# Optimization experiments

Hardware: AMD Instinct MI355X
Metric: run time of the kernel (lower is better)

## Reference

```python
import jax, jax.numpy as jnp
import numpy as np

H = 8  # num_heads
LN_EPS = 1e-5


def setup_inputs() -> dict:
    key = jax.random.key(0)
    ks = jax.random.split(key, 12)
    B, N, D = 1, 4096, 256
    E = 65536
    x = jax.random.normal(ks[0], (B, N, D), dtype=jnp.float32)
    # random edges + self-loops so every row of the mask has >=1 True (avoids NaN softmax)
    src = jax.random.randint(ks[1], (E,), 0, N)
    dst = jax.random.randint(ks[2], (E,), 0, N)
    loop = jnp.arange(N)
    edge_index = jnp.stack([jnp.concatenate([src, loop]),
                            jnp.concatenate([dst, loop])]).astype(jnp.int64)  # [2, 69632]
    s = 1.0 / np.sqrt(D)
    Wq = jax.random.normal(ks[3], (D, D), dtype=jnp.float32) * s
    Wk = jax.random.normal(ks[4], (D, D), dtype=jnp.float32) * s
    Wv = jax.random.normal(ks[5], (D, D), dtype=jnp.float32) * s
    Wo = jax.random.normal(ks[6], (D, D), dtype=jnp.float32) * s
    bq = jax.random.normal(ks[7], (D,), dtype=jnp.float32) * 0.01
    bk = jax.random.normal(ks[8], (D,), dtype=jnp.float32) * 0.01
    bv = jax.random.normal(ks[9], (D,), dtype=jnp.float32) * 0.01
    bo = jax.random.normal(ks[10], (D,), dtype=jnp.float32) * 0.01
    gamma = jnp.ones((D,), dtype=jnp.float32)
    beta = jnp.zeros((D,), dtype=jnp.float32)
    return {"x": x, "edge_index": edge_index, "Wq": Wq, "bq": bq, "Wk": Wk, "bk": bk,
            "Wv": Wv, "bv": bv, "Wo": Wo, "bo": bo, "gamma": gamma, "beta": beta}


def reference(x, edge_index, Wq, bq, Wk, bk, Wv, bv, Wo, bo, gamma, beta):
    B, N, D = x.shape
    hd = D // H
    # QKV projections -> [B, H, N, hd]
    def proj(W, b):
        return (x @ W + b).reshape(B, N, H, hd).transpose(0, 2, 1, 3)
    Q, K, V = proj(Wq, bq), proj(Wk, bk), proj(Wv, bv)
    scores = jnp.einsum('bhnd,bhmd->bhnm', Q, K) / jnp.sqrt(jnp.float32(hd))
    # dense boolean adjacency mask scattered from edge list
    mask = jnp.zeros((N, N), dtype=bool).at[edge_index[0], edge_index[1]].set(True)
    scores = jnp.where(mask[None, None], scores, -jnp.inf)
    attn = jax.nn.softmax(scores, axis=-1)  # dropout is identity in eval mode
    attended = jnp.einsum('bhnm,bhmd->bhnd', attn, V)
    attended = attended.transpose(0, 2, 1, 3).reshape(B, N, D)
    out = attended @ Wo + bo
    y = x + out
    mu = jnp.mean(y, axis=-1, keepdims=True)
    var = jnp.mean((y - mu) ** 2, axis=-1, keepdims=True)
    return (y - mu) / jnp.sqrt(var + LN_EPS) * gamma + beta
```

## Files before the change

kernel.cpp:

```cpp
#include <hip/hip_runtime.h>

#define N_NODES 4096
#define DMODEL  256
#define NHEAD   8
#define HDIM    32
#define LN_EPS  1e-5f
#define MAXDEG  64

typedef __attribute__((ext_vector_type(8))) short short8;
typedef __attribute__((ext_vector_type(4))) float f32x4;

__device__ __forceinline__ unsigned short f2bf(float f) {
  unsigned int x = __float_as_uint(f);
  x += 0x7fffu + ((x >> 16) & 1u);
  return (unsigned short)(x >> 16);
}
__device__ __forceinline__ float bf2f(unsigned short u) {
  return __uint_as_float(((unsigned int)u) << 16);
}

__device__ __forceinline__ int wt_off(int n, int k) {
  return ((k >> 5) * 4 + ((k >> 3) & 3)) * 2048 + n * 8 + (k & 7);
}

__global__ __launch_bounds__(256) void prep_kernel(
    const float* __restrict__ w0, const float* __restrict__ w1,
    const float* __restrict__ w2, const float* __restrict__ w3,
    unsigned short* __restrict__ wt,
    const int* __restrict__ e0, const int* __restrict__ e1, int ne, int eb,
    unsigned int* __restrict__ bits, int* __restrict__ cnt) {
  __shared__ float t[32][33];
  int bid = blockIdx.x, tid = threadIdx.x;
  if (bid < 256) {
    int kbi = bid & 7, nbi = (bid >> 3) & 7, m = bid >> 6;
    const float* w = (m == 0) ? w0 : (m == 1) ? w1 : (m == 2) ? w2 : w3;
    int tx = tid & 31, ty = tid >> 5;
    int kb = kbi * 32, nb = nbi * 32;
#pragma unroll
    for (int r = 0; r < 32; r += 8)
      t[ty + r][tx] = w[(kb + ty + r) * 256 + nb + tx];
    __syncthreads();
    unsigned short* o = wt + m * 65536;
#pragma unroll
    for (int r = 0; r < 32; r += 8)
      o[(kbi * 4 + (tx >> 3)) * 2048 + (nb + ty + r) * 8 + (tx & 7)] =
          f2bf(t[tx][ty + r]);
  } else if (bid < 256 + eb) {
    int i = (bid - 256) * 256 + tid;
    if (i < ne) {
      unsigned int bitpos = ((unsigned int)e0[i] << 12) | (unsigned int)e1[i];
      bits[bitpos >> 5] = 0u;
    }
  } else {
    cnt[(bid - 256 - eb) * 256 + tid] = 0;
  }
}

__global__ __launch_bounds__(512) void qkv_scatter(
    const float* __restrict__ x, const unsigned short* __restrict__ wt,
    const float* __restrict__ bq, const float* __restrict__ bk,
    const float* __restrict__ bv,
    const int* __restrict__ e0, const int* __restrict__ e1, int ne,
    unsigned int* __restrict__ bits, int* __restrict__ cnt,
    int* __restrict__ colidx,
    unsigned short* __restrict__ Qb, unsigned short* __restrict__ Kb,
    unsigned short* __restrict__ Vb) {
  int bid = blockIdx.x, tid = threadIdx.x;
  if (bid >= 256) {
    int i = (bid - 256) * 512 + tid;
    if (i < ne) {
      int s = e0[i], d = e1[i];
      unsigned int bitpos = ((unsigned int)s << 12) | (unsigned int)d;
      unsigned int word = bitpos >> 5, msk = 1u << (bitpos & 31);
      unsigned int old = atomicOr(&bits[word], msk);
      if (!(old & msk)) {
        int pos = atomicAdd(&cnt[s], 1);
        if (pos < MAXDEG) colidx[s * MAXDEG + pos] = d;
      }
    }
    return;
  }
  int lane = tid & 63, w = tid >> 6;
  int Mbase = bid * 16;
  int arow = lane & 15, kgrp = lane >> 4;
  short8 a[8];
  const float* ab = x + (Mbase + arow) * 256 + kgrp * 8;
#pragma unroll
  for (int kk = 0; kk < 8; ++kk) {
    float4 v0 = *reinterpret_cast<const float4*>(ab + kk * 32);
    float4 v1 = *reinterpret_cast<const float4*>(ab + kk * 32 + 4);
    short8 tv;
    tv[0] = (short)f2bf(v0.x); tv[1] = (short)f2bf(v0.y);
    tv[2] = (short)f2bf(v0.z); tv[3] = (short)f2bf(v0.w);
    tv[4] = (short)f2bf(v1.x); tv[5] = (short)f2bf(v1.y);
    tv[6] = (short)f2bf(v1.z); tv[7] = (short)f2bf(v1.w);
    a[kk] = tv;
  }
#pragma unroll
  for (int mat = 0; mat < 3; ++mat) {
    const unsigned short* wm = wt + mat * 65536;
    const float* bias_p = (mat == 0) ? bq : (mat == 1) ? bk : bv;
    unsigned short* o = (mat == 0) ? Qb : (mat == 1) ? Kb : Vb;
#pragma unroll
    for (int nf = 0; nf < 2; ++nf) {
      int col = w * 32 + nf * 16 + arow;
      const unsigned short* bb = wm + kgrp * 2048 + col * 8;
      f32x4 acc = {0.f, 0.f, 0.f, 0.f};
#pragma unroll
      for (int kk = 0; kk < 8; ++kk) {
        short8 b = *reinterpret_cast<const short8*>(bb + kk * 8192);
        acc = __builtin_amdgcn_mfma_f32_16x16x32_bf16(a[kk], b, acc, 0, 0, 0);
      }
      float bias = bias_p[col];
#pragma unroll
      for (int r = 0; r < 4; ++r) {
        int row = Mbase + kgrp * 4 + r;
        o[row * 256 + col] = f2bf(acc[r] + bias);
      }
    }
  }
}

__global__ __launch_bounds__(1024, 1) void attn_out_ln(
    const unsigned short* __restrict__ Qb, const unsigned short* __restrict__ Kb,
    const unsigned short* __restrict__ Vb, const int* __restrict__ cnt,
    const int* __restrict__ colidx, const unsigned short* __restrict__ wot,
    const float* __restrict__ bo, const float* __restrict__ x,
    const float* __restrict__ gamma, const float* __restrict__ beta,
    float* __restrict__ out) {
  __shared__ unsigned short att_lds[16][264];
  __shared__ float ylds[16][260];
  __shared__ float ps[16][65], pq[16][65];
  __shared__ float mu_s[16], ri_s[16];

  int tid = threadIdx.x;
  int Mbase = blockIdx.x * 16;
  const float scale = 0.17677669529663687f;

  {
    int g = tid >> 3;
    int gl = tid & 7;
    int ni = g >> 3, h = g & 7;
    int n = Mbase + ni;

    float qf[32];
    {
      const short8* q8 = reinterpret_cast<const short8*>(Qb + n * 256 + h * 32);
#pragma unroll
      for (int b = 0; b < 4; ++b) {
        short8 qv = q8[b];
#pragma unroll
        for (int j = 0; j < 8; ++j) qf[b * 8 + j] = bf2f((unsigned short)qv[j]) * scale;
      }
    }

    int deg = cnt[n]; deg = (deg > MAXDEG) ? MAXDEG : deg;
    const int* nbrs = colidx + n * MAXDEG;

    float s[8]; int c[8];
#pragma unroll
    for (int i = 0; i < 8; ++i) { s[i] = -3.0e38f; c[i] = 0; }
#pragma unroll
    for (int i = 0; i < 8; ++i) {
      if (8 * i >= deg) break;
      int idx = 8 * i + gl;
      if (idx < deg) {
        c[i] = nbrs[idx];
        const short8* k8 = reinterpret_cast<const short8*>(Kb + c[i] * 256 + h * 32);
        float d = 0.f;
#pragma unroll
        for (int b = 0; b < 4; ++b) {
          short8 kv = k8[b];
#pragma unroll
          for (int j = 0; j < 8; ++j)
            d += qf[b * 8 + j] * bf2f((unsigned short)kv[j]);
        }
        s[i] = d;
      }
    }

    float gm = s[0];
#pragma unroll
    for (int i = 1; i < 8; ++i) gm = fmaxf(gm, s[i]);
    gm = fmaxf(gm, __shfl_xor(gm, 1, 8));
    gm = fmaxf(gm, __shfl_xor(gm, 2, 8));
    gm = fmaxf(gm, __shfl_xor(gm, 4, 8));

    float l = 0.f;
#pragma unroll
    for (int i = 0; i < 8; ++i) {
      if (8 * i >= deg) break;
      s[i] = __expf(s[i] - gm);
      l += s[i];
    }
    l += __shfl_xor(l, 1, 8);
    l += __shfl_xor(l, 2, 8);
    l += __shfl_xor(l, 4, 8);

    float a0 = 0.f, a1 = 0.f, a2 = 0.f, a3 = 0.f;
#pragma unroll
    for (int i = 0; i < 8; ++i) {
      if (8 * i >= deg) break;
#pragma unroll
      for (int lj = 0; lj < 8; ++lj) {
        if (8 * i + lj >= deg) break;
        float pj = __shfl(s[i], lj, 8);
        int cj = __shfl(c[i], lj, 8);
        ushort4 vv = *reinterpret_cast<const ushort4*>(Vb + cj * 256 + h * 32 + gl * 4);
        a0 += pj * bf2f(vv.x);
        a1 += pj * bf2f(vv.y);
        a2 += pj * bf2f(vv.z);
        a3 += pj * bf2f(vv.w);
      }
    }
    float rl = 1.f / l;
    ushort4 pkt;
    pkt.x = f2bf(a0 * rl); pkt.y = f2bf(a1 * rl);
    pkt.z = f2bf(a2 * rl); pkt.w = f2bf(a3 * rl);
    *reinterpret_cast<ushort4*>(&att_lds[ni][h * 32 + gl * 4]) = pkt;
  }
  __syncthreads();

  {
    int lane = tid & 63, w = tid >> 6;
    int arow = lane & 15, kgrp = lane >> 4;

    short8 a[8];
#pragma unroll
    for (int kk = 0; kk < 8; ++kk)
      a[kk] = *reinterpret_cast<const short8*>(&att_lds[arow][kgrp * 8 + kk * 32]);

    int col = w * 16 + arow;
    const unsigned short* bb = wot + kgrp * 2048 + col * 8;
    f32x4 acc = {0.f, 0.f, 0.f, 0.f};
#pragma unroll
    for (int kk = 0; kk < 8; ++kk) {
      short8 b = *reinterpret_cast<const short8*>(bb + kk * 8192);
      acc = __builtin_amdgcn_mfma_f32_16x16x32_bf16(a[kk], b, acc, 0, 0, 0);
    }
    float bof = bo[col];
#pragma unroll
    for (int r = 0; r < 4; ++r) {
      int row = kgrp * 4 + r;
      float xv = x[(Mbase + row) * 256 + col];
      ylds[row][col] = acc[r] + bof + xv;
    }
  }
  __syncthreads();

  int r = tid >> 6, seg = tid & 63;
  float sm = 0.f, sq = 0.f;
#pragma unroll
  for (int j = 0; j < 4; ++j) {
    float v = ylds[r][seg * 4 + j];
    sm += v;
    sq += v * v;
  }
  ps[r][seg] = sm;
  pq[r][seg] = sq;
  __syncthreads();
  if (tid < 16) {
    float S = 0.f, Q2 = 0.f;
#pragma unroll
    for (int cc = 0; cc < 64; ++cc) { S += ps[tid][cc]; Q2 += pq[tid][cc]; }
    float mu = S * (1.f / 256.f);
    float var = Q2 * (1.f / 256.f) - mu * mu;
    mu_s[tid] = mu;
    ri_s[tid] = rsqrtf(var + LN_EPS);
  }
  __syncthreads();
  float mu = mu_s[r], ri = ri_s[r];
  float* orow = out + (Mbase + r) * 256;
#pragma unroll
  for (int j = 0; j < 4; ++j) {
    int cc = seg * 4 + j;
    float v = (ylds[r][cc] - mu) * ri * gamma[cc] + beta[cc];
    orow[cc] = v;
  }
}

extern "C" void kernel_launch(void* const* d_in, const int* in_sizes, int n_in,
                              void* d_out, int out_size, void* d_ws, size_t ws_size,
                              hipStream_t stream) {
  const float* x     = (const float*)d_in[0];
  const int*   edges = (const int*)d_in[1];
  const float* Wq    = (const float*)d_in[2];
  const float* bq    = (const float*)d_in[3];
  const float* Wk    = (const float*)d_in[4];
  const float* bk    = (const float*)d_in[5];
  const float* Wv    = (const float*)d_in[6];
  const float* bv    = (const float*)d_in[7];
  const float* Wo    = (const float*)d_in[8];
  const float* bo    = (const float*)d_in[9];
  const float* gamma = (const float*)d_in[10];
  const float* beta  = (const float*)d_in[11];
  float* out = (float*)d_out;
  int NE = in_sizes[1] / 2;
  int EB256 = (NE + 255) / 256;
  int EB512 = (NE + 511) / 512;

  char* p = (char*)d_ws;
  auto carve = [&](size_t sz) { char* r = p; p += ((sz + 255) / 256) * 256; return r; };
  unsigned short* Wt   = (unsigned short*)carve(4 * 65536 * sizeof(unsigned short));
  unsigned short* Qb   = (unsigned short*)carve((size_t)N_NODES * DMODEL * sizeof(unsigned short));
  unsigned short* Kb   = (unsigned short*)carve((size_t)N_NODES * DMODEL * sizeof(unsigned short));
  unsigned short* Vb   = (unsigned short*)carve((size_t)N_NODES * DMODEL * sizeof(unsigned short));
  unsigned int*   bits = (unsigned int*)carve((size_t)N_NODES * N_NODES / 8);
  int*            cnt  = (int*)carve(N_NODES * sizeof(int));
  int*            colidx = (int*)carve((size_t)N_NODES * MAXDEG * sizeof(int));

  prep_kernel<<<256 + EB256 + 16, 256, 0, stream>>>(Wq, Wk, Wv, Wo, Wt,
                                                    edges, edges + NE, NE, EB256, bits, cnt);
  qkv_scatter<<<256 + EB512, 512, 0, stream>>>(x, Wt, bq, bk, bv,
                                               edges, edges + NE, NE, bits, cnt, colidx,
                                               Qb, Kb, Vb);
  attn_out_ln<<<256, 1024, 0, stream>>>(Qb, Kb, Vb, cnt, colidx, Wt + 3 * 65536,
                                        bo, x, gamma, beta, out);
}
```

Baseline: 48.88 us.

## Fuse three kernels into one persistent kernel with grid-wide barriers

Merges the weight-transpose/clear, QKV projection plus edge scatter, and attention plus output projection plus LayerNorm kernels into a single 256-block launch. Grid-wide atomic counter barriers separate the stages, and a memset resets the counter before launch. This removes two kernel launch gaps and their tail effects. In exchange it depends on all 256 blocks being co-resident, and the per-block work is redistributed, with each wave now computing one column tile per matrix.

Result: slower. 124.6 us (+155.0%).

```diff
diff --git a/kernel.cpp b/kernel.cpp
--- a/kernel.cpp
+++ b/kernel.cpp
@@ -19,263 +19,267 @@
   return __uint_as_float(((unsigned int)u) << 16);
 }
 
-__device__ __forceinline__ int wt_off(int n, int k) {
-  return ((k >> 5) * 4 + ((k >> 3) & 3)) * 2048 + n * 8 + (k & 7);
-}
-
-__global__ __launch_bounds__(256) void prep_kernel(
-    const float* __restrict__ w0, const float* __restrict__ w1,
-    const float* __restrict__ w2, const float* __restrict__ w3,
-    unsigned short* __restrict__ wt,
-    const int* __restrict__ e0, const int* __restrict__ e1, int ne, int eb,
-    unsigned int* __restrict__ bits, int* __restrict__ cnt) {
+__device__ __forceinline__ void gbar(unsigned int* ctr, unsigned int target) {
+  __syncthreads();
+  if (threadIdx.x == 0) {
+    __threadfence();
+    __hip_atomic_fetch_add(ctr, 1u, __ATOMIC_SEQ_CST, __HIP_MEMORY_SCOPE_AGENT);
+    while (__hip_atomic_load(ctr, __ATOMIC_SEQ_CST, __HIP_MEMORY_SCOPE_AGENT) < target)
+      __builtin_amdgcn_s_sleep(8);
+    __threadfence();
+  }
+  __syncthreads();
+}
+
+__global__ __launch_bounds__(1024, 1) void fused_all(
+    const float* __restrict__ x, const int* __restrict__ edges, int ne,
+    const float* __restrict__ Wq, const float* __restrict__ bq,
+    const float* __restrict__ Wk, const float* __restrict__ bk,
+    const float* __restrict__ Wv, const float* __restrict__ bv,
+    const float* __restrict__ Wo, const float* __restrict__ bo,
+    const float* __restrict__ gamma, const float* __restrict__ beta,
+    unsigned short* wt, unsigned short* Qb, unsigned short* Kb,
+    unsigned short* Vb, unsigned int* bits, int* cnt, int* colidx,
+    unsigned int* ctr, float* __restrict__ out) {
   __shared__ float t[32][33];
-  int bid = blockIdx.x, tid = threadIdx.x;
-  if (bid < 256) {
-    int kbi = bid & 7, nbi = (bid >> 3) & 7, m = bid >> 6;
-    const float* w = (m == 0) ? w0 : (m == 1) ? w1 : (m == 2) ? w2 : w3;
-    int tx = tid & 31, ty = tid >> 5;
-    int kb = kbi * 32, nb = nbi * 32;
-#pragma unroll
-    for (int r = 0; r < 32; r += 8)
-      t[ty + r][tx] = w[(kb + ty + r) * 256 + nb + tx];
-    __syncthreads();
-    unsigned short* o = wt + m * 65536;
-#pragma unroll
-    for (int r = 0; r < 32; r += 8)
-      o[(kbi * 4 + (tx >> 3)) * 2048 + (nb + ty + r) * 8 + (tx & 7)] =
-          f2bf(t[tx][ty + r]);
-  } else if (bid < 256 + eb) {
-    int i = (bid - 256) * 256 + tid;
-    if (i < ne) {
-      unsigned int bitpos = ((unsigned int)e0[i] << 12) | (unsigned int)e1[i];
-      bits[bitpos >> 5] = 0u;
-    }
-  } else {
-    cnt[(bid - 256 - eb) * 256 + tid] = 0;
-  }
-}
-
-__global__ __launch_bounds__(512) void qkv_scatter(
-    const float* __restrict__ x, const unsigned short* __restrict__ wt,
-    const float* __restrict__ bq, const float* __restrict__ bk,
-    const float* __restrict__ bv,
-    const int* __restrict__ e0, const int* __restrict__ e1, int ne,
-    unsigned int* __restrict__ bits, int* __restrict__ cnt,
-    int* __restrict__ colidx,
-    unsigned short* __restrict__ Qb, unsigned short* __restrict__ Kb,
-    unsigned short* __restrict__ Vb) {
-  int bid = blockIdx.x, tid = threadIdx.x;
-  if (bid >= 256) {
-    int i = (bid - 256) * 512 + tid;
-    if (i < ne) {
-      int s = e0[i], d = e1[i];
-      unsigned int bitpos = ((unsigned int)s << 12) | (unsigned int)d;
-      unsigned int word = bitpos >> 5, msk = 1u << (bitpos & 31);
-      unsigned int old = atomicOr(&bits[word], msk);
-      if (!(old & msk)) {
-        int pos = atomicAdd(&cnt[s], 1);
-        if (pos < MAXDEG) colidx[s * MAXDEG + pos] = d;
-      }
-    }
-    return;
-  }
-  int lane = tid & 63, w = tid >> 6;
-  int Mbase = bid * 16;
-  int arow = lane & 15, kgrp = lane >> 4;
-  short8 a[8];
-  const float* ab = x + (Mbase + arow) * 256 + kgrp * 8;
-#pragma unroll
-  for (int kk = 0; kk < 8; ++kk) {
-    float4 v0 = *reinterpret_cast<const float4*>(ab + kk * 32);
-    float4 v1 = *reinterpret_cast<const float4*>(ab + kk * 32 + 4);
-    short8 tv;
-    tv[0] = (short)f2bf(v0.x); tv[1] = (short)f2bf(v0.y);
-    tv[2] = (short)f2bf(v0.z); tv[3] = (short)f2bf(v0.w);
-    tv[4] = (short)f2bf(v1.x); tv[5] = (short)f2bf(v1.y);
-    tv[6] = (short)f2bf(v1.z); tv[7] = (short)f2bf(v1.w);
-    a[kk] = tv;
-  }
-#pragma unroll
-  for (int mat = 0; mat < 3; ++mat) {
-    const unsigned short* wm = wt + mat * 65536;
-    const float* bias_p = (mat == 0) ? bq : (mat == 1) ? bk : bv;
-    unsigned short* o = (mat == 0) ? Qb : (mat == 1) ? Kb : Vb;
-#pragma unroll
-    for (int nf = 0; nf < 2; ++nf) {
-      int col = w * 32 + nf * 16 + arow;
-      const unsigned short* bb = wm + kgrp * 2048 + col * 8;
-      f32x4 acc = {0.f, 0.f, 0.f, 0.f};
-#pragma unroll
-      for (int kk = 0; kk < 8; ++kk) {
-        short8 b = *reinterpret_cast<const short8*>(bb + kk * 8192);
-        acc = __builtin_amdgcn_mfma_f32_16x16x32_bf16(a[kk], b, acc, 0, 0, 0);
-      }
-      float bias = bias_p[col];
-#pragma unroll
-      for (int r = 0; r < 4; ++r) {
-        int row = Mbase + kgrp * 4 + r;
-        o[row * 256 + col] = f2bf(acc[r] + bias);
-      }
-    }
-  }
-}
-
-__global__ __launch_bounds__(1024, 1) void attn_out_ln(
-    const unsigned short* __restrict__ Qb, const unsigned short* __restrict__ Kb,
-    const unsigned short* __restrict__ Vb, const int* __restrict__ cnt,
-    const int* __restrict__ colidx, const unsigned short* __restrict__ wot,
-    const float* __restrict__ bo, const float* __restrict__ x,
-    const float* __restrict__ gamma, const float* __restrict__ beta,
-    float* __restrict__ out) {
   __shared__ unsigned short att_lds[16][264];
   __shared__ float ylds[16][260];
   __shared__ float ps[16][65], pq[16][65];
   __shared__ float mu_s[16], ri_s[16];
 
-  int tid = threadIdx.x;
-  int Mbase = blockIdx.x * 16;
+  const int tid = threadIdx.x;
+  const int bid = blockIdx.x;
+  const int* e0 = edges;
+  const int* e1 = edges + ne;
   const float scale = 0.17677669529663687f;
 
   {
-    int g = tid >> 3;
-    int gl = tid & 7;
-    int ni = g >> 3, h = g & 7;
-    int n = Mbase + ni;
-
-    float qf[32];
-    {
-      const short8* q8 = reinterpret_cast<const short8*>(Qb + n * 256 + h * 32);
-#pragma unroll
-      for (int b = 0; b < 4; ++b) {
-        short8 qv = q8[b];
-#pragma unroll
-        for (int j = 0; j < 8; ++j) qf[b * 8 + j] = bf2f((unsigned short)qv[j]) * scale;
-      }
-    }
-
-    int deg = cnt[n]; deg = (deg > MAXDEG) ? MAXDEG : deg;
-    const int* nbrs = colidx + n * MAXDEG;
-
-    float s[8]; int c[8];
-#pragma unroll
-    for (int i = 0; i < 8; ++i) { s[i] = -3.0e38f; c[i] = 0; }
-#pragma unroll
-    for (int i = 0; i < 8; ++i) {
-      if (8 * i >= deg) break;
-      int idx = 8 * i + gl;
-      if (idx < deg) {
-        c[i] = nbrs[idx];
-        const short8* k8 = reinterpret_cast<const short8*>(Kb + c[i] * 256 + h * 32);
-        float d = 0.f;
-#pragma unroll
-        for (int b = 0; b < 4; ++b) {
-          short8 kv = k8[b];
-#pragma unroll
-          for (int j = 0; j < 8; ++j)
-            d += qf[b * 8 + j] * bf2f((unsigned short)kv[j]);
-        }
-        s[i] = d;
-      }
-    }
-
-    float gm = s[0];
-#pragma unroll
-    for (int i = 1; i < 8; ++i) gm = fmaxf(gm, s[i]);
-    gm = fmaxf(gm, __shfl_xor(gm, 1, 8));
-    gm = fmaxf(gm, __shfl_xor(gm, 2, 8));
-    gm = fmaxf(gm, __shfl_xor(gm, 4, 8));
-
-    float l = 0.f;
-#pragma unroll
-    for (int i = 0; i < 8; ++i) {
-      if (8 * i >= deg) break;
-      s[i] = __expf(s[i] - gm);
-      l += s[i];
-    }
-    l += __shfl_xor(l, 1, 8);
-    l += __shfl_xor(l, 2, 8);
-    l += __shfl_xor(l, 4, 8);
-
-    float a0 = 0.f, a1 = 0.f, a2 = 0.f, a3 = 0.f;
-#pragma unroll
-    for (int i = 0; i < 8; ++i) {
-      if (8 * i >= deg) break;
-#pragma unroll
-      for (int lj = 0; lj < 8; ++lj) {
-        if (8 * i + lj >= deg) break;
-        float pj = __shfl(s[i], lj, 8);
-        int cj = __shfl(c[i], lj, 8);
-        ushort4 vv = *reinterpret_cast<const ushort4*>(Vb + cj * 256 + h * 32 + gl * 4);
-        a0 += pj * bf2f(vv.x);
-        a1 += pj * bf2f(vv.y);
-        a2 += pj * bf2f(vv.z);
-        a3 += pj * bf2f(vv.w);
-      }
-    }
-    float rl = 1.f / l;
-    ushort4 pkt;
-    pkt.x = f2bf(a0 * rl); pkt.y = f2bf(a1 * rl);
-    pkt.z = f2bf(a2 * rl); pkt.w = f2bf(a3 * rl);
-    *reinterpret_cast<ushort4*>(&att_lds[ni][h * 32 + gl * 4]) = pkt;
+    int kbi = bid & 7, nbi = (bid >> 3) & 7, m = bid >> 6;
+    const float* w = (m == 0) ? Wq : (m == 1) ? Wk : (m == 2) ? Wv : Wo;
+    int kb = kbi * 32, nb = nbi * 32;
+    if (tid < 256) {
+      int tx = tid & 31, ty = tid >> 5;
+#pragma unroll
+      for (int r = 0; r < 32; r += 8)
+        t[ty + r][tx] = w[(kb + ty + r) * 256 + nb + tx];
+    } else {
+      int j = bid * 768 + (tid - 256);
+      if (j < ne) {
+        unsigned int bitpos = ((unsigned int)e0[j] << 12) | (unsigned int)e1[j];
+        bits[bitpos >> 5] = 0u;
+      }
+      if (j < N_NODES) cnt[j] = 0;
+    }
+    __syncthreads();
+    if (tid < 256) {
+      int tx = tid & 31, ty = tid >> 5;
+      unsigned short* o = wt + m * 65536;
+#pragma unroll
+      for (int r = 0; r < 32; r += 8)
+        o[(kbi * 4 + (tx >> 3)) * 2048 + (nb + ty + r) * 8 + (tx & 7)] =
+            f2bf(t[tx][ty + r]);
+    }
   }
-  __syncthreads();
+  gbar(ctr, 256);
 
   {
     int lane = tid & 63, w = tid >> 6;
+    int Mbase = bid * 16;
     int arow = lane & 15, kgrp = lane >> 4;
-
     short8 a[8];
-#pragma unroll
-    for (int kk = 0; kk < 8; ++kk)
-      a[kk] = *reinterpret_cast<const short8*>(&att_lds[arow][kgrp * 8 + kk * 32]);
-
-    int col = w * 16 + arow;
-    const unsigned short* bb = wot + kgrp * 2048 + col * 8;
-    f32x4 acc = {0.f, 0.f, 0.f, 0.f};
+    const float* ab = x + (Mbase + arow) * 256 + kgrp * 8;
 #pragma unroll
     for (int kk = 0; kk < 8; ++kk) {
-      short8 b = *reinterpret_cast<const short8*>(bb + kk * 8192);
-      acc = __builtin_amdgcn_mfma_f32_16x16x32_bf16(a[kk], b, acc, 0, 0, 0);
-    }
-    float bof = bo[col];
-#pragma unroll
-    for (int r = 0; r < 4; ++r) {
-      int row = kgrp * 4 + r;
-      float xv = x[(Mbase + row) * 256 + col];
-      ylds[row][col] = acc[r] + bof + xv;
+      float4 v0 = *reinterpret_cast<const float4*>(ab + kk * 32);
+      float4 v1 = *reinterpret_cast<const float4*>(ab + kk * 32 + 4);
+      short8 tv;
+      tv[0] = (short)f2bf(v0.x); tv[1] = (short)f2bf(v0.y);
+      tv[2] = (short)f2bf(v0.z); tv[3] = (short)f2bf(v0.w);
+      tv[4] = (short)f2bf(v1.x); tv[5] = (short)f2bf(v1.y);
+      tv[6] = (short)f2bf(v1.z); tv[7] = (short)f2bf(v1.w);
+      a[kk] = tv;
+    }
+#pragma unroll
+    for (int mat = 0; mat < 3; ++mat) {
+      const unsigned short* wm = wt + mat * 65536;
+      const float* bias_p = (mat == 0) ? bq : (mat == 1) ? bk : bv;
+      unsigned short* o = (mat == 0) ? Qb : (mat == 1) ? Kb : Vb;
+      int col = w * 16 + arow;
+      const unsigned short* bb = wm + kgrp * 2048 + col * 8;
+      f32x4 acc = {0.f, 0.f, 0.f, 0.f};
+#pragma unroll
+      for (int kk = 0; kk < 8; ++kk) {
+        short8 b = *reinterpret_cast<const short8*>(bb + kk * 8192);
+        acc = __builtin_amdgcn_mfma_f32_16x16x32_bf16(a[kk], b, acc, 0, 0, 0);
+      }
+      float bias = bias_p[col];
+#pragma unroll
+      for (int r = 0; r < 4; ++r) {
+        int row = Mbase + kgrp * 4 + r;
+        o[row * 256 + col] = f2bf(acc[r] + bias);
+      }
+    }
+    int epb = (ne + 255) >> 8;
+    for (int tt = tid; tt < epb; tt += 1024) {
+      int i = bid * epb + tt;
+      if (i < ne) {
+        int s = e0[i], d = e1[i];
+        unsigned int bitpos = ((unsigned int)s << 12) | (unsigned int)d;
+        unsigned int word = bitpos >> 5, msk = 1u << (bitpos & 31);
+        unsigned int old = atomicOr(&bits[word], msk);
+        if (!(old & msk)) {
+          int pos = atomicAdd(&cnt[s], 1);
+          if (pos < MAXDEG) colidx[s * MAXDEG + pos] = d;
+        }
+      }
     }
   }
-  __syncthreads();
-
-  int r = tid >> 6, seg = tid & 63;
-  float sm = 0.f, sq = 0.f;
-#pragma unroll
-  for (int j = 0; j < 4; ++j) {
-    float v = ylds[r][seg * 4 + j];
-    sm += v;
-    sq += v * v;
-  }
-  ps[r][seg] = sm;
-  pq[r][seg] = sq;
-  __syncthreads();
-  if (tid < 16) {
-    float S = 0.f, Q2 = 0.f;
-#pragma unroll
-    for (int cc = 0; cc < 64; ++cc) { S += ps[tid][cc]; Q2 += pq[tid][cc]; }
-    float mu = S * (1.f / 256.f);
-    float var = Q2 * (1.f / 256.f) - mu * mu;
-    mu_s[tid] = mu;
-    ri_s[tid] = rsqrtf(var + LN_EPS);
-  }
-  __syncthreads();
-  float mu = mu_s[r], ri = ri_s[r];
-  float* orow = out + (Mbase + r) * 256;
-#pragma unroll
-  for (int j = 0; j < 4; ++j) {
-    int cc = seg * 4 + j;
-    float v = (ylds[r][cc] - mu) * ri * gamma[cc] + beta[cc];
-    orow[cc] = v;
+  gbar(ctr, 512);
+
+  {
+    int Mbase = bid * 16;
+    {
+      int g = tid >> 3;
+      int gl = tid & 7;
+      int ni = g >> 3, h = g & 7;
+      int n = Mbase + ni;
+
+      float qf[32];
+      {
+        const short8* q8 = reinterpret_cast<const short8*>(Qb + n * 256 + h * 32);
+#pragma unroll
+        for (int b = 0; b < 4; ++b) {
+          short8 qv = q8[b];
+#pragma unroll
+          for (int j = 0; j < 8; ++j)
+            qf[b * 8 + j] = bf2f((unsigned short)qv[j]) * scale;
+        }
+      }
+
+      int deg = cnt[n]; deg = (deg > MAXDEG) ? MAXDEG : deg;
+      const int* nbrs = colidx + n * MAXDEG;
+
+      float s[8]; int c[8];
+#pragma unroll
+      for (int i = 0; i < 8; ++i) { s[i] = -3.0e38f; c[i] = 0; }
+#pragma unroll
+      for (int i = 0; i < 8; ++i) {
+        if (8 * i >= deg) break;
+        int idx = 8 * i + gl;
+        if (idx < deg) {
+          c[i] = nbrs[idx];
+          const short8* k8 = reinterpret_cast<const short8*>(Kb + c[i] * 256 + h * 32);
+          float d = 0.f;
+#pragma unroll
+          for (int b = 0; b < 4; ++b) {
+            short8 kv = k8[b];
+#pragma unroll
+            for (int j = 0; j < 8; ++j)
+              d += qf[b * 8 + j] * bf2f((unsigned short)kv[j]);
+          }
+          s[i] = d;
+        }
+      }
+
+      float gm = s[0];
+#pragma unroll
+      for (int i = 1; i < 8; ++i) gm = fmaxf(gm, s[i]);
+      gm = fmaxf(gm, __shfl_xor(gm, 1, 8));
+      gm = fmaxf(gm, __shfl_xor(gm, 2, 8));
+      gm = fmaxf(gm, __shfl_xor(gm, 4, 8));
+
+      float l = 0.f;
+#pragma unroll
+      for (int i = 0; i < 8; ++i) {
+        if (8 * i >= deg) break;
+        s[i] = __expf(s[i] - gm);
+        l += s[i];
+      }
+      l += __shfl_xor(l, 1, 8);
+      l += __shfl_xor(l, 2, 8);
+      l += __shfl_xor(l, 4, 8);
+
+      float a0 = 0.f, a1 = 0.f, a2 = 0.f, a3 = 0.f;
+#pragma unroll
+      for (int i = 0; i < 8; ++i) {
+        if (8 * i >= deg) break;
+#pragma unroll
+        for (int lj = 0; lj < 8; ++lj) {
+          if (8 * i + lj >= deg) break;
+          float pj = __shfl(s[i], lj, 8);
+          int cj = __shfl(c[i], lj, 8);
+          ushort4 vv = *reinterpret_cast<const ushort4*>(Vb + cj * 256 + h * 32 + gl * 4);
+          a0 += pj * bf2f(vv.x);
+          a1 += pj * bf2f(vv.y);
+          a2 += pj * bf2f(vv.z);
+          a3 += pj * bf2f(vv.w);
+        }
+      }
+      float rl = 1.f / l;
+      ushort4 pkt;
+      pkt.x = f2bf(a0 * rl); pkt.y = f2bf(a1 * rl);
+      pkt.z = f2bf(a2 * rl); pkt.w = f2bf(a3 * rl);
+      *reinterpret_cast<ushort4*>(&att_lds[ni][h * 32 + gl * 4]) = pkt;
+    }
+    __syncthreads();
+
+    {
+      int lane = tid & 63, w = tid >> 6;
+      int arow = lane & 15, kgrp = lane >> 4;
+      const unsigned short* wot = wt + 3 * 65536;
+
+      short8 a[8];
+#pragma unroll
+      for (int kk = 0; kk < 8; ++kk)
+        a[kk] = *reinterpret_cast<const short8*>(&att_lds[arow][kgrp * 8 + kk * 32]);
+
+      int col = w * 16 + arow;
+      const unsigned short* bb = wot + kgrp * 2048 + col * 8;
+      f32x4 acc = {0.f, 0.f, 0.f, 0.f};
+#pragma unroll
+      for (int kk = 0; kk < 8; ++kk) {
+        short8 b = *reinterpret_cast<const short8*>(bb + kk * 8192);
+        acc = __builtin_amdgcn_mfma_f32_16x16x32_bf16(a[kk], b, acc, 0, 0, 0);
+      }
+      float bof = bo[col];
+#pragma unroll
+      for (int r = 0; r < 4; ++r) {
+        int row = kgrp * 4 + r;
+        float xv = x[(Mbase + row) * 256 + col];
+        ylds[row][col] = acc[r] + bof + xv;
+      }
+    }
+    __syncthreads();
+
+    int r = tid >> 6, seg = tid & 63;
+    float sm = 0.f, sq = 0.f;
+#pragma unroll
+    for (int j = 0; j < 4; ++j) {
+      float v = ylds[r][seg * 4 + j];
+      sm += v;
+      sq += v * v;
+    }
+    ps[r][seg] = sm;
+    pq[r][seg] = sq;
+    __syncthreads();
+    if (tid < 16) {
+      float S = 0.f, Q2 = 0.f;
+#pragma unroll
+      for (int cc = 0; cc < 64; ++cc) { S += ps[tid][cc]; Q2 += pq[tid][cc]; }
+      float mu = S * (1.f / 256.f);
+      float var = Q2 * (1.f / 256.f) - mu * mu;
+      mu_s[tid] = mu;
+      ri_s[tid] = rsqrtf(var + LN_EPS);
+    }
+    __syncthreads();
+    float mu = mu_s[r], ri = ri_s[r];
+    float* orow = out + (Mbase + r) * 256;
+#pragma unroll
+    for (int j = 0; j < 4; ++j) {
+      int cc = seg * 4 + j;
+      float v = (ylds[r][cc] - mu) * ri * gamma[cc] + beta[cc];
+      orow[cc] = v;
+    }
   }
 }
 
@@ -296,8 +300,6 @@
   const float* beta  = (const float*)d_in[11];
   float* out = (float*)d_out;
   int NE = in_sizes[1] / 2;
-  int EB256 = (NE + 255) / 256;
-  int EB512 = (NE + 511) / 512;
 
   char* p = (char*)d_ws;
   auto carve = [&](size_t sz) { char* r = p; p += ((sz + 255) / 256) * 256; return r; };
@@ -308,12 +310,10 @@
   unsigned int*   bits = (unsigned int*)carve((size_t)N_NODES * N_NODES / 8);
   int*            cnt  = (int*)carve(N_NODES * sizeof(int));
   int*            colidx = (int*)carve((size_t)N_NODES * MAXDEG * sizeof(int));
-
-  prep_kernel<<<256 + EB256 + 16, 256, 0, stream>>>(Wq, Wk, Wv, Wo, Wt,
-                                                    edges, edges + NE, NE, EB256, bits, cnt);
-  qkv_scatter<<<256 + EB512, 512, 0, stream>>>(x, Wt, bq, bk, bv,
-                                               edges, edges + NE, NE, bits, cnt, colidx,
-                                               Qb, Kb, Vb);
-  attn_out_ln<<<256, 1024, 0, stream>>>(Qb, Kb, Vb, cnt, colidx, Wt + 3 * 65536,
-                                        bo, x, gamma, beta, out);
-}
+  unsigned int*   ctr  = (unsigned int*)carve(256);
+
+  hipMemsetAsync(ctr, 0, sizeof(unsigned int), stream);
+  fused_all<<<256, 1024, 0, stream>>>(x, edges, NE, Wq, bq, Wk, bk, Wv, bv,
+                                      Wo, bo, gamma, beta, Wt, Qb, Kb, Vb,
+                                      bits, cnt, colidx, ctr, out);
+}
```

## Build CSR adjacency per 64-row block in shared memory instead of global bitmap

Applied to the files above, without the earlier changes.

Replaces the global 2MB dedup bitmap, its clearing pass and the global atomics with 64 blocks that each scan the full edge list. Each block keeps a 64x4096 bitmap and per-row counters in LDS for its 64 source nodes. This removes global atomic traffic and the zeroing work in prep_kernel. In exchange every CSR block reads all ~70K edges, and the kernel now uses 32KB of LDS, which may lower occupancy for the QKV GEMM blocks that share it.

New measurement: 93.24 us. +90.8%, slower.

```diff
diff --git a/kernel.cpp b/kernel.cpp
--- a/kernel.cpp
+++ b/kernel.cpp
@@ -19,67 +19,62 @@
   return __uint_as_float(((unsigned int)u) << 16);
 }
 
-__device__ __forceinline__ int wt_off(int n, int k) {
-  return ((k >> 5) * 4 + ((k >> 3) & 3)) * 2048 + n * 8 + (k & 7);
-}
-
 __global__ __launch_bounds__(256) void prep_kernel(
     const float* __restrict__ w0, const float* __restrict__ w1,
     const float* __restrict__ w2, const float* __restrict__ w3,
-    unsigned short* __restrict__ wt,
-    const int* __restrict__ e0, const int* __restrict__ e1, int ne, int eb,
-    unsigned int* __restrict__ bits, int* __restrict__ cnt) {
+    unsigned short* __restrict__ wt) {
   __shared__ float t[32][33];
   int bid = blockIdx.x, tid = threadIdx.x;
-  if (bid < 256) {
-    int kbi = bid & 7, nbi = (bid >> 3) & 7, m = bid >> 6;
-    const float* w = (m == 0) ? w0 : (m == 1) ? w1 : (m == 2) ? w2 : w3;
-    int tx = tid & 31, ty = tid >> 5;
-    int kb = kbi * 32, nb = nbi * 32;
-#pragma unroll
-    for (int r = 0; r < 32; r += 8)
-      t[ty + r][tx] = w[(kb + ty + r) * 256 + nb + tx];
-    __syncthreads();
-    unsigned short* o = wt + m * 65536;
-#pragma unroll
-    for (int r = 0; r < 32; r += 8)
-      o[(kbi * 4 + (tx >> 3)) * 2048 + (nb + ty + r) * 8 + (tx & 7)] =
-          f2bf(t[tx][ty + r]);
-  } else if (bid < 256 + eb) {
-    int i = (bid - 256) * 256 + tid;
-    if (i < ne) {
-      unsigned int bitpos = ((unsigned int)e0[i] << 12) | (unsigned int)e1[i];
-      bits[bitpos >> 5] = 0u;
-    }
-  } else {
-    cnt[(bid - 256 - eb) * 256 + tid] = 0;
-  }
-}
-
-__global__ __launch_bounds__(512) void qkv_scatter(
+  int kbi = bid & 7, nbi = (bid >> 3) & 7, m = bid >> 6;
+  const float* w = (m == 0) ? w0 : (m == 1) ? w1 : (m == 2) ? w2 : w3;
+  int tx = tid & 31, ty = tid >> 5;
+  int kb = kbi * 32, nb = nbi * 32;
+#pragma unroll
+  for (int r = 0; r < 32; r += 8)
+    t[ty + r][tx] = w[(kb + ty + r) * 256 + nb + tx];
+  __syncthreads();
+  unsigned short* o = wt + m * 65536;
+#pragma unroll
+  for (int r = 0; r < 32; r += 8)
+    o[(kbi * 4 + (tx >> 3)) * 2048 + (nb + ty + r) * 8 + (tx & 7)] =
+        f2bf(t[tx][ty + r]);
+}
+
+__global__ __launch_bounds__(512) void qkv_csr(
     const float* __restrict__ x, const unsigned short* __restrict__ wt,
     const float* __restrict__ bq, const float* __restrict__ bk,
     const float* __restrict__ bv,
     const int* __restrict__ e0, const int* __restrict__ e1, int ne,
-    unsigned int* __restrict__ bits, int* __restrict__ cnt,
-    int* __restrict__ colidx,
+    int* __restrict__ cnt, int* __restrict__ colidx,
     unsigned short* __restrict__ Qb, unsigned short* __restrict__ Kb,
     unsigned short* __restrict__ Vb) {
+  __shared__ unsigned int bm[64 * 128];
+  __shared__ int lcnt[64];
   int bid = blockIdx.x, tid = threadIdx.x;
+
   if (bid >= 256) {
-    int i = (bid - 256) * 512 + tid;
-    if (i < ne) {
-      int s = e0[i], d = e1[i];
-      unsigned int bitpos = ((unsigned int)s << 12) | (unsigned int)d;
-      unsigned int word = bitpos >> 5, msk = 1u << (bitpos & 31);
-      unsigned int old = atomicOr(&bits[word], msk);
-      if (!(old & msk)) {
-        int pos = atomicAdd(&cnt[s], 1);
-        if (pos < MAXDEG) colidx[s * MAXDEG + pos] = d;
-      }
-    }
+    int cb = bid - 256;
+    for (int i = tid; i < 64 * 128; i += 512) bm[i] = 0u;
+    if (tid < 64) lcnt[tid] = 0;
+    __syncthreads();
+    for (int i = tid; i < ne; i += 512) {
+      int s = e0[i];
+      if ((s >> 6) == cb) {
+        int d = e1[i];
+        int li = s & 63;
+        unsigned int msk = 1u << (d & 31);
+        unsigned int old = atomicOr(&bm[li * 128 + (d >> 5)], msk);
+        if (!(old & msk)) {
+          int pos = atomicAdd(&lcnt[li], 1);
+          if (pos < MAXDEG) colidx[s * MAXDEG + pos] = d;
+        }
+      }
+    }
+    __syncthreads();
+    if (tid < 64) cnt[cb * 64 + tid] = lcnt[tid];
     return;
   }
+
   int lane = tid & 63, w = tid >> 6;
   int Mbase = bid * 16;
   int arow = lane & 15, kgrp = lane >> 4;
@@ -150,7 +145,8 @@
       for (int b = 0; b < 4; ++b) {
         short8 qv = q8[b];
 #pragma unroll
-        for (int j = 0; j < 8; ++j) qf[b * 8 + j] = bf2f((unsigned short)qv[j]) * scale;
+        for (int j = 0; j < 8; ++j)
+          qf[b * 8 + j] = bf2f((unsigned short)qv[j]) * scale;
       }
     }
 
@@ -296,8 +292,6 @@
   const float* beta  = (const float*)d_in[11];
   float* out = (float*)d_out;
   int NE = in_sizes[1] / 2;
-  int EB256 = (NE + 255) / 256;
-  int EB512 = (NE + 511) / 512;
 
   char* p = (char*)d_ws;
   auto carve = [&](size_t sz) { char* r = p; p += ((sz + 255) / 256) * 256; return r; };
@@ -305,15 +299,13 @@
   unsigned short* Qb   = (unsigned short*)carve((size_t)N_NODES * DMODEL * sizeof(unsigned short));
   unsigned short* Kb   = (unsigned short*)carve((size_t)N_NODES * DMODEL * sizeof(unsigned short));
   unsigned short* Vb   = (unsigned short*)carve((size_t)N_NODES * DMODEL * sizeof(unsigned short));
-  unsigned int*   bits = (unsigned int*)carve((size_t)N_NODES * N_NODES / 8);
   int*            cnt  = (int*)carve(N_NODES * sizeof(int));
   int*            colidx = (int*)carve((size_t)N_NODES * MAXDEG * sizeof(int));
 
-  prep_kernel<<<256 + EB256 + 16, 256, 0, stream>>>(Wq, Wk, Wv, Wo, Wt,
-                                                    edges, edges + NE, NE, EB256, bits, cnt);
-  qkv_scatter<<<256 + EB512, 512, 0, stream>>>(x, Wt, bq, bk, bv,
-                                               edges, edges + NE, NE, bits, cnt, colidx,
-                                               Qb, Kb, Vb);
+  prep_kernel<<<256, 256, 0, stream>>>(Wq, Wk, Wv, Wo, Wt);
+  qkv_csr<<<320, 512, 0, stream>>>(x, Wt, bq, bk, bv,
+                                   edges, edges + NE, NE, cnt, colidx,
+                                   Qb, Kb, Vb);
   attn_out_ln<<<256, 1024, 0, stream>>>(Qb, Kb, Vb, cnt, colidx, Wt + 3 * 65536,
                                         bo, x, gamma, beta, out);
 }
```
